# Kernel optimization log

Measured on AMD Instinct MI355X. Metric: run time of the kernel, lower is better.

Reference implementation:

```python
import jax, jax.numpy as jnp
import numpy as np


def setup_inputs() -> dict:
    key = jax.random.key(0)
    k1, k2 = jax.random.split(key)
    B, T, D, P = 32, 8192, 128, 1024
    mel = jax.random.normal(k1, (B, T, D), dtype=jnp.float32)
    # durations in [0, 9); max possible sum = P*8 = T, so slices never overrun
    duration = jax.random.randint(k2, (B, P), 0, 9, dtype=jnp.int64)
    return {"mel": mel, "duration": duration}


def reference(mel, duration):
    # mel: (B, T, D) float; duration: (B, P) int, consumed sequentially.
    B, T, D = mel.shape
    P = duration.shape[1]
    ends = jnp.cumsum(duration, axis=1)  # (B, P): exclusive end frame of each phoneme
    t = jnp.arange(T)
    # segment id of frame t = first phoneme whose end > t; frames past sum(d) map to P
    seg = jax.vmap(lambda e: jnp.searchsorted(e, t, side="right"))(ends)  # (B, T)
    sums = jax.vmap(
        lambda m, s: jax.ops.segment_sum(m, s, num_segments=P + 1)
    )(mel, seg)[:, :P]  # (B, P, D), dropping the overflow bucket
    d = duration.astype(mel.dtype)[..., None]  # (B, P, 1)
    # mean over each phoneme's frames; zeros where duration == 0 (matches torch init)
    return jnp.where(d > 0, sums / jnp.maximum(d, 1), jnp.zeros((), mel.dtype))
```

## Files before the change

kernel.cpp:

```cpp
#include <hip/hip_runtime.h>

#define BB 32
#define TT 8192
#define DD 128
#define PP 1024

__global__ void __launch_bounds__(256)
phoneme_fused_kernel(const float* __restrict__ mel,
                     const int* __restrict__ dur,
                     float* __restrict__ out) {
    __shared__ int sh[256];
    __shared__ int starts_sh[PP];

    const int b    = blockIdx.x >> 7;
    const int pblk = blockIdx.x & 127;
    const int t    = threadIdx.x;

    const int4 v = ((const int4*)(dur + b * PP))[t];
    const int local = v.x + v.y + v.z + v.w;

    sh[t] = local;
    __syncthreads();

    #pragma unroll
    for (int off = 1; off < 256; off <<= 1) {
        int other = (t >= off) ? sh[t - off] : 0;
        __syncthreads();
        sh[t] += other;
        __syncthreads();
    }
    const int excl = sh[t] - local;

    starts_sh[4 * t + 0] = excl;
    starts_sh[4 * t + 1] = excl + v.x;
    starts_sh[4 * t + 2] = excl + v.x + v.y;
    starts_sh[4 * t + 3] = excl + v.x + v.y + v.z;
    __syncthreads();

    const int r    = t >> 5;
    const int lane = t & 31;
    const int p    = pblk * 8 + r;

    const int s = starts_sh[p];
    const int d = dur[b * PP + p];

    const float4* base =
        (const float4*)(mel + ((size_t)b * TT + (size_t)s) * DD) + lane;

    float4 acc[8];
    #pragma unroll
    for (int k = 0; k < 8; ++k) {
        acc[k] = make_float4(0.f, 0.f, 0.f, 0.f);
        if (k < d) acc[k] = base[k * (DD / 4)];
    }

    #pragma unroll
    for (int off = 4; off >= 1; off >>= 1) {
        #pragma unroll
        for (int k = 0; k < off; ++k) {
            acc[k].x += acc[k + off].x;
            acc[k].y += acc[k + off].y;
            acc[k].z += acc[k + off].z;
            acc[k].w += acc[k + off].w;
        }
    }

    const float inv = (d > 0) ? (1.0f / (float)d) : 0.0f;
    acc[0].x *= inv; acc[0].y *= inv; acc[0].z *= inv; acc[0].w *= inv;

    ((float4*)out)[((size_t)b * PP + p) * (DD / 4) + lane] = acc[0];
}

extern "C" void kernel_launch(void* const* d_in, const int* in_sizes, int n_in,
                              void* d_out, int out_size, void* d_ws, size_t ws_size,
                              hipStream_t stream) {
    const float* mel = (const float*)d_in[0];
    const int*   dur = (const int*)d_in[1];
    float*       out = (float*)d_out;

    phoneme_fused_kernel<<<(BB * PP) / 8, 256, 0, stream>>>(mel, dur, out);
}
```

Baseline: 180.1 us.

## Use wave-shuffle prefix scan, 512-thread blocks, and cache durations in LDS

Replaces the barrier-heavy shared-memory Hillis-Steele scan with a 64-lane shuffle scan plus a small per-wave total combine, so only two block barriers are needed. Blocks grow to 512 threads covering 16 phonemes each, which halves the number of blocks that redo the per-batch duration scan. Durations are also kept in LDS, avoiding a second global load. The larger blocks may lower scheduling flexibility, but the kernel is mostly bandwidth bound on mel reads.

```diff
diff --git a/kernel.cpp b/kernel.cpp
--- a/kernel.cpp
+++ b/kernel.cpp
@@ -5,44 +5,52 @@
 #define DD 128
 #define PP 1024
 
-__global__ void __launch_bounds__(256)
+__global__ void __launch_bounds__(512)
 phoneme_fused_kernel(const float* __restrict__ mel,
                      const int* __restrict__ dur,
                      float* __restrict__ out) {
-    __shared__ int sh[256];
+    __shared__ int wave_tot[8];
     __shared__ int starts_sh[PP];
+    __shared__ int dur_sh[PP];
 
-    const int b    = blockIdx.x >> 7;
-    const int pblk = blockIdx.x & 127;
-    const int t    = threadIdx.x;
+    const int b      = blockIdx.x >> 6;
+    const int pblk   = blockIdx.x & 63;
+    const int t      = threadIdx.x;
+    const int wave   = t >> 6;
+    const int lane64 = t & 63;
 
-    const int4 v = ((const int4*)(dur + b * PP))[t];
-    const int local = v.x + v.y + v.z + v.w;
+    const int2 v = ((const int2*)(dur + b * PP))[t];
+    const int tsum = v.x + v.y;
 
-    sh[t] = local;
+    int scan = tsum;
+    #pragma unroll
+    for (int off = 1; off < 64; off <<= 1) {
+        int up = __shfl_up(scan, off, 64);
+        if (lane64 >= off) scan += up;
+    }
+    if (lane64 == 63) wave_tot[wave] = scan;
     __syncthreads();
 
+    int wave_prefix = 0;
     #pragma unroll
-    for (int off = 1; off < 256; off <<= 1) {
-        int other = (t >= off) ? sh[t - off] : 0;
-        __syncthreads();
-        sh[t] += other;
-        __syncthreads();
+    for (int w = 0; w < 7; ++w) {
+        int wt = wave_tot[w];
+        if (w < wave) wave_prefix += wt;
     }
-    const int excl = sh[t] - local;
 
-    starts_sh[4 * t + 0] = excl;
-    starts_sh[4 * t + 1] = excl + v.x;
-    starts_sh[4 * t + 2] = excl + v.x + v.y;
-    starts_sh[4 * t + 3] = excl + v.x + v.y + v.z;
+    const int excl = wave_prefix + (scan - tsum);
+    starts_sh[2 * t]     = excl;
+    starts_sh[2 * t + 1] = excl + v.x;
+    dur_sh[2 * t]        = v.x;
+    dur_sh[2 * t + 1]    = v.y;
     __syncthreads();
 
     const int r    = t >> 5;
     const int lane = t & 31;
-    const int p    = pblk * 8 + r;
+    const int p    = pblk * 16 + r;
 
     const int s = starts_sh[p];
-    const int d = dur[b * PP + p];
+    const int d = dur_sh[p];
 
     const float4* base =
         (const float4*)(mel + ((size_t)b * TT + (size_t)s) * DD) + lane;
@@ -78,5 +86,5 @@
     const int*   dur = (const int*)d_in[1];
     float*       out = (float*)d_out;
 
-    phoneme_fused_kernel<<<(BB * PP) / 8, 256, 0, stream>>>(mel, dur, out);
+    phoneme_fused_kernel<<<(BB * PP) / 16, 512, 0, stream>>>(mel, dur, out);
 }
```

After: 180.1 us. No clear change (-0.0%).
